# Optimization experiments

Measured on AMD Instinct MI355X. Metric: run time of the kernel, lower is better.

Reference implementation:

```python
import jax, jax.numpy as jnp
import numpy as np

H = 8            # num_heads
A = 8            # num_atlas
LAMBDA_INIT = 0.8
EPS = 1e-5


def setup_inputs() -> dict:
    key = jax.random.key(0)
    ks = jax.random.split(key, 12)
    B, N, D = 16, 2048, 1024
    d = D // (2 * H)  # half-head dim = 64
    sc = D ** -0.5
    return {
        "x": jax.random.normal(ks[0], (B, N, D), jnp.float32),
        "atlas_q": jax.random.normal(ks[1], (A, D), jnp.float32) * 0.02,  # learned atlas query tokens
        "Wq": jax.random.normal(ks[2], (D, D), jnp.float32) * sc,
        "Wk": jax.random.normal(ks[3], (D, D), jnp.float32) * sc,
        "Wv": jax.random.normal(ks[4], (D, D), jnp.float32) * sc,
        "Wo": jax.random.normal(ks[5], (D, D), jnp.float32) * sc,
        "rms_w": jnp.ones((2 * d,), jnp.float32),
        "Whead": jax.random.normal(ks[6], (D, 1), jnp.float32) * sc,
        "lq1": jax.random.normal(ks[7], (d,), jnp.float32) * 0.1,
        "lk1": jax.random.normal(ks[8], (d,), jnp.float32) * 0.1,
        "lq2": jax.random.normal(ks[9], (d,), jnp.float32) * 0.1,
        "lk2": jax.random.normal(ks[10], (d,), jnp.float32) * 0.1,
    }


def reference(x, atlas_q, Wq, Wk, Wv, Wo, rms_w, Whead, lq1, lk1, lq2, lk2):
    B, N, D = x.shape
    d = D // (2 * H)
    # projections (bias-free, as in DIFF transformer)
    q = (atlas_q @ Wq).reshape(A, 2 * H, d)          # [A, 2H, d]
    k = (x @ Wk).reshape(B, N, 2 * H, d)             # [B, N, 2H, d]
    v = (x @ Wv).reshape(B, N, H, 2 * d)             # [B, N, H, 2d]
    # attention scores: atlas queries attend over tokens
    scores = jnp.einsum("ahd,bnhd->bhan", q, k) * (d ** -0.5)  # [B, 2H, A, N]
    s = jax.nn.softmax(scores, axis=-1).reshape(B, H, 2, A, N)
    # differential lambda
    lam = jnp.exp(jnp.dot(lq1, lk1)) - jnp.exp(jnp.dot(lq2, lk2)) + LAMBDA_INIT
    diff = s[:, :, 0] - lam * s[:, :, 1]             # [B, H, A, N]
    out = jnp.einsum("bhan,bnhe->bahe", diff, v)     # [B, A, H, 2d]
    # per-head RMSNorm, scaled by (1 - lambda_init)
    out = out * jax.lax.rsqrt(jnp.mean(out * out, axis=-1, keepdims=True) + EPS)
    out = out * rms_w * (1.0 - LAMBDA_INIT)
    out = out.reshape(B, A, D) @ Wo                  # [B, A, D]
    logits = (out @ Whead)[..., 0]                   # [B, A] routing logits
    return logits
```

## Files before the change

kernel.cpp:

```cpp
#include <hip/hip_runtime.h>
#include <hip/hip_bf16.h>
#include <cstdint>

#define BB 16
#define NN 2048
#define DD 1024
#define HH 8
#define AA 8
#define CC 128
#define DH 64
#define TD 128
#define LAMBDA_INIT 0.8f
#define EPS_ 1e-5f

typedef short short8 __attribute__((ext_vector_type(8)));
typedef float f32x4  __attribute__((ext_vector_type(4)));

static __device__ __forceinline__ ushort f2bf(float f) {
    uint32_t u = __float_as_uint(f);
    return (ushort)((u + 0x8000u) >> 16);
}

static constexpr size_t OFF_QPROJP = 0;
static constexpr size_t OFF_M2     = 65536;
static constexpr size_t OFF_LAM    = 131072;
static constexpr size_t OFF_WOH    = 131136;
static constexpr size_t OFF_SC     = 132160;
static constexpr size_t OFF_DIFFB  = OFF_SC + 4194304;

__global__ __launch_bounds__(256) void k_setup(const float* __restrict__ atlas_q,
                                               const float* __restrict__ Wq,
                                               const float* __restrict__ Wo,
                                               const float* __restrict__ Whead,
                                               const float* __restrict__ lq1,
                                               const float* __restrict__ lk1,
                                               const float* __restrict__ lq2,
                                               const float* __restrict__ lk2,
                                               float* __restrict__ qprojp,
                                               float* __restrict__ woh,
                                               float* __restrict__ lam) {
    int blk = blockIdx.x;
    int tid = threadIdx.x;
    if (blk < 128) {
        __shared__ float aqS[8][128];
        __shared__ float redS[4][8][64];
        int jt = blk >> 3, iq = blk & 7;
        if (tid < 128) {
#pragma unroll
            for (int a = 0; a < 8; ++a) aqS[a][tid] = atlas_q[a * DD + iq * 128 + tid];
        }
        __syncthreads();
        int jl = tid & 63, is = tid >> 6;
        float acc[8] = {};
        const float* wq = Wq + (size_t)(iq * 128 + is * 32) * DD + jt * 64 + jl;
#pragma unroll 8
        for (int ii = 0; ii < 32; ++ii) {
            float wv = wq[(size_t)ii * DD];
            int i = is * 32 + ii;
#pragma unroll
            for (int a = 0; a < 8; ++a) acc[a] = fmaf(aqS[a][i], wv, acc[a]);
        }
#pragma unroll
        for (int a = 0; a < 8; ++a) redS[is][a][jl] = acc[a];
        __syncthreads();
        if (tid < 64) {
#pragma unroll
            for (int a = 0; a < 8; ++a)
                qprojp[(size_t)iq * 8192 + a * 1024 + jt * 64 + tid] =
                    redS[0][a][tid] + redS[1][a][tid] + redS[2][a][tid] + redS[3][a][tid];
        }
    } else if (blk < 192) {
        int i0 = (blk - 128) * 16;
        int il = tid >> 4, jt = tid & 15;
        const float* row = Wo + (size_t)(i0 + il) * DD;
        float acc = 0.f;
#pragma unroll 4
        for (int u = 0; u < 16; ++u) {
            float4 r  = *(const float4*)(row + u * 64 + jt * 4);
            float4 wv = *(const float4*)(Whead + u * 64 + jt * 4);
            acc += r.x * wv.x + r.y * wv.y + r.z * wv.z + r.w * wv.w;
        }
#pragma unroll
        for (int off = 8; off; off >>= 1) acc += __shfl_down(acc, off);
        if ((tid & 15) == 0) woh[i0 + il] = acc;
    } else {
        if (tid < 64) {
            float p1 = lq1[tid] * lk1[tid];
            float p2 = lq2[tid] * lk2[tid];
#pragma unroll
            for (int off = 32; off; off >>= 1) {
                p1 += __shfl_down(p1, off);
                p2 += __shfl_down(p2, off);
            }
            if (tid == 0) *lam = expf(p1) - expf(p2) + LAMBDA_INIT;
        }
    }
}

__global__ __launch_bounds__(256) void k_m2(const float* __restrict__ qprojp,
                                            const float* __restrict__ Wk,
                                            ushort* __restrict__ M2) {
    __shared__ float qpS[8192];
    int jb = blockIdx.x;
    int tid = threadIdx.x;
#pragma unroll
    for (int e = 0; e < 32; ++e) {
        int idx = tid + e * 256;
        float s = 0.f;
#pragma unroll
        for (int iq = 0; iq < 8; ++iq) s += qprojp[(size_t)iq * 8192 + idx];
        qpS[idx] = s;
    }
    __syncthreads();
    int h2 = tid >> 4;
#pragma unroll
    for (int jr = 0; jr < 2; ++jr) {
        int j = jb * 2 + jr;
        float4 wv = *(const float4*)(Wk + (size_t)j * DD + tid * 4);
        float p[8];
#pragma unroll
        for (int a = 0; a < 8; ++a) {
            float4 q4 = *(const float4*)(&qpS[a * DD + tid * 4]);
            p[a] = q4.x * wv.x + q4.y * wv.y + q4.z * wv.z + q4.w * wv.w;
        }
#pragma unroll
        for (int off = 8; off; off >>= 1)
#pragma unroll
            for (int a = 0; a < 8; ++a) p[a] += __shfl_down(p[a], off);
        if ((tid & 15) == 0) {
#pragma unroll
            for (int a = 0; a < 8; ++a)
                M2[(size_t)(h2 * 8 + a) * DD + j] = f2bf(p[a] * 0.125f);
        }
    }
}

__global__ __launch_bounds__(256, 4) void k_scores(const float* __restrict__ x,
                                                   const ushort* __restrict__ M2,
                                                   float* __restrict__ scores) {
    int b = blockIdx.x, nt = blockIdx.y;
    int tid = threadIdx.x;
    int lane = tid & 63, w = tid >> 6;
    int wn = w >> 1, wc = w & 1;
    int l15 = lane & 15, kg = lane >> 4;
    int n = nt * 32 + wn * 16 + l15;
    const float* xr = x + ((size_t)b * NN + n) * DD + kg * 8;

    f32x4 acc[4] = {};
    float4 pa0 = *(const float4*)(xr);
    float4 pa1 = *(const float4*)(xr + 4);
    float4 pa2 = *(const float4*)(xr + 32);
    float4 pa3 = *(const float4*)(xr + 36);

    for (int j0 = 0; j0 < DD; j0 += 64) {
        float4 ca0 = pa0, ca1 = pa1, ca2 = pa2, ca3 = pa3;
        if (j0 < DD - 64) {
            pa0 = *(const float4*)(xr + j0 + 64);
            pa1 = *(const float4*)(xr + j0 + 68);
            pa2 = *(const float4*)(xr + j0 + 96);
            pa3 = *(const float4*)(xr + j0 + 100);
        }
        short8 av0, av1;
        av0[0] = (short)f2bf(ca0.x); av0[1] = (short)f2bf(ca0.y);
        av0[2] = (short)f2bf(ca0.z); av0[3] = (short)f2bf(ca0.w);
        av0[4] = (short)f2bf(ca1.x); av0[5] = (short)f2bf(ca1.y);
        av0[6] = (short)f2bf(ca1.z); av0[7] = (short)f2bf(ca1.w);
        av1[0] = (short)f2bf(ca2.x); av1[1] = (short)f2bf(ca2.y);
        av1[2] = (short)f2bf(ca2.z); av1[3] = (short)f2bf(ca2.w);
        av1[4] = (short)f2bf(ca3.x); av1[5] = (short)f2bf(ca3.y);
        av1[6] = (short)f2bf(ca3.z); av1[7] = (short)f2bf(ca3.w);
        const ushort* m2b = M2 + (size_t)(wc * 64) * DD + j0 + kg * 8;
#pragma unroll
        for (int ct = 0; ct < 4; ++ct) {
            uint4 b0 = *(const uint4*)(m2b + (size_t)(ct * 16 + l15) * DD);
            uint4 b1 = *(const uint4*)(m2b + (size_t)(ct * 16 + l15) * DD + 32);
            acc[ct] = __builtin_amdgcn_mfma_f32_16x16x32_bf16(
                av0, __builtin_bit_cast(short8, b0), acc[ct], 0, 0, 0);
            acc[ct] = __builtin_amdgcn_mfma_f32_16x16x32_bf16(
                av1, __builtin_bit_cast(short8, b1), acc[ct], 0, 0, 0);
        }
    }
#pragma unroll
    for (int ct = 0; ct < 4; ++ct) {
        int c = wc * 64 + ct * 16 + l15;
        float4 o = {acc[ct][0], acc[ct][1], acc[ct][2], acc[ct][3]};
        *(float4*)(scores + ((size_t)b * CC + c) * NN + nt * 32 + wn * 16 + kg * 4) = o;
    }
}

__global__ __launch_bounds__(256) void k_softdiff(const float* __restrict__ scores,
                                                  const float* __restrict__ lam_p,
                                                  ushort* __restrict__ diffb) {
    int blk = blockIdx.x;
    int b = blk >> 6, h = (blk >> 3) & 7, a = blk & 7;
    int tid = threadIdx.x;
    const float* r0 = scores + ((size_t)b * CC + (2 * h) * AA + a) * NN;
    const float* r1 = scores + ((size_t)b * CC + (2 * h + 1) * AA + a) * NN;
    float v0[8], v1[8];
    float m0 = -1e30f, m1 = -1e30f;
#pragma unroll
    for (int k = 0; k < 8; ++k) {
        v0[k] = r0[tid + k * 256];
        v1[k] = r1[tid + k * 256];
        m0 = fmaxf(m0, v0[k]); m1 = fmaxf(m1, v1[k]);
    }
    __shared__ float redm[4][2];
    __shared__ float reds[4][2];
    int w = tid >> 6, lane = tid & 63;
#pragma unroll
    for (int off = 32; off; off >>= 1) {
        m0 = fmaxf(m0, __shfl_down(m0, off));
        m1 = fmaxf(m1, __shfl_down(m1, off));
    }
    if (lane == 0) { redm[w][0] = m0; redm[w][1] = m1; }
    __syncthreads();
    m0 = fmaxf(fmaxf(redm[0][0], redm[1][0]), fmaxf(redm[2][0], redm[3][0]));
    m1 = fmaxf(fmaxf(redm[0][1], redm[1][1]), fmaxf(redm[2][1], redm[3][1]));
    float s0 = 0.f, s1 = 0.f;
#pragma unroll
    for (int k = 0; k < 8; ++k) {
        v0[k] = expf(v0[k] - m0); s0 += v0[k];
        v1[k] = expf(v1[k] - m1); s1 += v1[k];
    }
#pragma unroll
    for (int off = 32; off; off >>= 1) {
        s0 += __shfl_down(s0, off);
        s1 += __shfl_down(s1, off);
    }
    if (lane == 0) { reds[w][0] = s0; reds[w][1] = s1; }
    __syncthreads();
    s0 = reds[0][0] + reds[1][0] + reds[2][0] + reds[3][0];
    s1 = reds[0][1] + reds[1][1] + reds[2][1] + reds[3][1];
    float lam = *lam_p;
    float inv0 = 1.f / s0;
    float inv1 = lam / s1;
    ushort* drow = diffb + ((size_t)b * 64 + a * 8 + h) * NN;
#pragma unroll
    for (int k = 0; k < 8; ++k)
        drow[tid + k * 256] = f2bf(v0[k] * inv0 - v1[k] * inv1);
}

__global__ __launch_bounds__(256, 4) void k_agg(const float* __restrict__ x,
                                                const ushort* __restrict__ diffb,
                                                float* __restrict__ aggp) {
    __shared__ ushort xT[64 * 32];
    int b = blockIdx.x, jt = blockIdx.y, sk = blockIdx.z;
    int j0 = jt * 64;
    int tid = threadIdx.x;
    int nl = tid & 31, jc = tid >> 5;
    int lane = tid & 63, w = tid >> 6;
    int l15 = lane & 15, kg = lane >> 4;
    int nbase = sk * 512;

    f32x4 acc[4] = {};
    const float* xb = x + (size_t)b * NN * DD;
    const ushort* drow = diffb + (size_t)b * 64 * NN;

    const float* s0p = xb + (size_t)(nbase + nl) * DD + j0 + jc * 8;
    float4 p0 = *(const float4*)(s0p);
    float4 p1 = *(const float4*)(s0p + 4);
    uint4 an[4];
#pragma unroll
    for (int rt = 0; rt < 4; ++rt)
        an[rt] = *(const uint4*)(drow + (size_t)(rt * 16 + l15) * NN + nbase + kg * 8);

    for (int stp = 0; stp < 16; ++stp) {
        int jb = jc * 8;
        xT[(jb + 0) * 32 + nl] = f2bf(p0.x);
        xT[(jb + 1) * 32 + nl] = f2bf(p0.y);
        xT[(jb + 2) * 32 + nl] = f2bf(p0.z);
        xT[(jb + 3) * 32 + nl] = f2bf(p0.w);
        xT[(jb + 4) * 32 + nl] = f2bf(p1.x);
        xT[(jb + 5) * 32 + nl] = f2bf(p1.y);
        xT[(jb + 6) * 32 + nl] = f2bf(p1.z);
        xT[(jb + 7) * 32 + nl] = f2bf(p1.w);
        uint4 ac0 = an[0], ac1 = an[1], ac2 = an[2], ac3 = an[3];
        if (stp < 15) {
            int n1 = nbase + (stp + 1) * 32;
            const float* sp = xb + (size_t)(n1 + nl) * DD + j0 + jc * 8;
            p0 = *(const float4*)(sp);
            p1 = *(const float4*)(sp + 4);
#pragma unroll
            for (int rt = 0; rt < 4; ++rt)
                an[rt] = *(const uint4*)(drow + (size_t)(rt * 16 + l15) * NN + n1 + kg * 8);
        }
        __syncthreads();
        short8 bv = __builtin_bit_cast(short8,
            *(const uint4*)(xT + (size_t)(w * 16 + l15) * 32 + kg * 8));
        acc[0] = __builtin_amdgcn_mfma_f32_16x16x32_bf16(__builtin_bit_cast(short8, ac0), bv, acc[0], 0, 0, 0);
        acc[1] = __builtin_amdgcn_mfma_f32_16x16x32_bf16(__builtin_bit_cast(short8, ac1), bv, acc[1], 0, 0, 0);
        acc[2] = __builtin_amdgcn_mfma_f32_16x16x32_bf16(__builtin_bit_cast(short8, ac2), bv, acc[2], 0, 0, 0);
        acc[3] = __builtin_amdgcn_mfma_f32_16x16x32_bf16(__builtin_bit_cast(short8, ac3), bv, acc[3], 0, 0, 0);
        __syncthreads();
    }
    int jj = j0 + w * 16 + l15;
#pragma unroll
    for (int rt = 0; rt < 4; ++rt) {
#pragma unroll
        for (int reg = 0; reg < 4; ++reg) {
            int r = rt * 16 + kg * 4 + reg;
            aggp[(((size_t)sk * BB + b) * 64 + r) * DD + jj] = acc[rt][reg];
        }
    }
}

__global__ __launch_bounds__(256) void k_yp(const float* __restrict__ aggp,
                                            const float* __restrict__ Wv,
                                            float* __restrict__ Y) {
    __shared__ float As[8][32];
    __shared__ float Ws[32][128];
    int h = blockIdx.x, rt = blockIdx.y;
    int tid = threadIdx.x;
    int rl = tid >> 5, te = tid & 31;
    int row0 = rt * 8;
    float a0 = 0.f, a1 = 0.f, a2 = 0.f, a3 = 0.f;
    for (int j0 = 0; j0 < DD; j0 += 32) {
        {
            int r = row0 + rl;
            int b_ = r >> 3, a_ = r & 7;
            size_t base = (((size_t)b_ * 64) + a_ * 8 + h) * DD + j0 + te;
            const size_t skS = (size_t)BB * 64 * DD;
            As[rl][te] = aggp[base] + aggp[base + skS] + aggp[base + 2 * skS] + aggp[base + 3 * skS];
        }
#pragma unroll
        for (int t = 0; t < 4; ++t) {
            int f4 = tid + t * 256;
            int jj = f4 >> 5, e4 = (f4 & 31) * 4;
            *(float4*)(&Ws[jj][e4]) = *(const float4*)(Wv + (size_t)(j0 + jj) * DD + h * TD + e4);
        }
        __syncthreads();
#pragma unroll
        for (int jj = 0; jj < 32; ++jj) {
            float av = As[rl][jj];
            float4 w4 = *(const float4*)(&Ws[jj][te * 4]);
            a0 = fmaf(av, w4.x, a0);
            a1 = fmaf(av, w4.y, a1);
            a2 = fmaf(av, w4.z, a2);
            a3 = fmaf(av, w4.w, a3);
        }
        __syncthreads();
    }
    float4 o = {a0, a1, a2, a3};
    *(float4*)(Y + (size_t)(row0 + rl) * DD + h * TD + te * 4) = o;
}

__global__ __launch_bounds__(256) void k_logits(const float* __restrict__ Y,
                                                const float* __restrict__ rms_w,
                                                const float* __restrict__ woh,
                                                float* __restrict__ logits) {
    int row = blockIdx.x;
    int tid = threadIdx.x;
    int w = tid >> 6, lane = tid & 63;
    __shared__ float hss[8];
    __shared__ float red[4];
    float y[4];
    if (tid < 8) hss[tid] = 0.f;
    __syncthreads();
#pragma unroll
    for (int k = 0; k < 4; ++k) {
        int p = k * 256 + tid;
        y[k] = Y[(size_t)row * DD + p];
        float s = y[k] * y[k];
#pragma unroll
        for (int off = 32; off; off >>= 1) s += __shfl_down(s, off);
        if (lane == 0) atomicAdd(&hss[(k * 256 + w * 64) >> 7], s);
    }
    __syncthreads();
    float val = 0.f;
#pragma unroll
    for (int k = 0; k < 4; ++k) {
        int p = k * 256 + tid;
        int hh = p >> 7, e = p & 127;
        float rs = rsqrtf(hss[hh] * (1.f / 128.f) + EPS_);
        val += y[k] * rs * rms_w[e] * (1.f - LAMBDA_INIT) * woh[p];
    }
#pragma unroll
    for (int off = 32; off; off >>= 1) val += __shfl_down(val, off);
    if (lane == 0) red[w] = val;
    __syncthreads();
    if (tid == 0) logits[row] = red[0] + red[1] + red[2] + red[3];
}

extern "C" void kernel_launch(void* const* d_in, const int* in_sizes, int n_in,
                              void* d_out, int out_size, void* d_ws, size_t ws_size,
                              hipStream_t stream) {
    (void)in_sizes; (void)n_in; (void)out_size; (void)ws_size;
    const float* x       = (const float*)d_in[0];
    const float* atlas_q = (const float*)d_in[1];
    const float* Wq      = (const float*)d_in[2];
    const float* Wk      = (const float*)d_in[3];
    const float* Wv      = (const float*)d_in[4];
    const float* Wo      = (const float*)d_in[5];
    const float* rms_w   = (const float*)d_in[6];
    const float* Whead   = (const float*)d_in[7];
    const float* lq1     = (const float*)d_in[8];
    const float* lk1     = (const float*)d_in[9];
    const float* lq2     = (const float*)d_in[10];
    const float* lk2     = (const float*)d_in[11];
    float* out = (float*)d_out;
    float* ws  = (float*)d_ws;

    float*  qprojp = ws + OFF_QPROJP;
    ushort* M2     = (ushort*)(ws + OFF_M2);
    float*  lam    = ws + OFF_LAM;
    float*  woh    = ws + OFF_WOH;
    float*  scores = ws + OFF_SC;
    float*  aggp   = ws + OFF_SC;
    ushort* diffb  = (ushort*)(ws + OFF_DIFFB);
    float*  Y      = ws + OFF_DIFFB;

    hipLaunchKernelGGL(k_setup,    dim3(193),       dim3(256), 0, stream,
                       atlas_q, Wq, Wo, Whead, lq1, lk1, lq2, lk2, qprojp, woh, lam);
    hipLaunchKernelGGL(k_m2,       dim3(512),       dim3(256), 0, stream, qprojp, Wk, M2);
    hipLaunchKernelGGL(k_scores,   dim3(16, 64),    dim3(256), 0, stream, x, M2, scores);
    hipLaunchKernelGGL(k_softdiff, dim3(1024),      dim3(256), 0, stream, scores, lam, diffb);
    hipLaunchKernelGGL(k_agg,      dim3(16, 16, 4), dim3(256), 0, stream, x, diffb, aggp);
    hipLaunchKernelGGL(k_yp,       dim3(8, 16),     dim3(256), 0, stream, aggp, Wv, Y);
    hipLaunchKernelGGL(k_logits,   dim3(128),       dim3(256), 0, stream, Y, rms_w, woh, out);
}
```

Baseline: 380.8 us.

## Stage x and M2 tiles through double-buffered LDS and split k_yp over j

k_scores now handles 64 token rows per block. It stages both the bf16-converted x tile and the M2 tile in padded, double-buffered shared memory, so each wave reuses the shared A and B fragments across 4x2 MFMA tiles instead of reloading M2 from global memory per wave. k_agg moves to 64-token chunks with a double-buffered transpose buffer and register prefetch of both operands, halving the number of barriers per MFMA. k_yp is split four ways along the reduction dimension for more parallelism, with the partial sums combined in k_logits. The changes add shared memory use and register pressure, which may lower occupancy.

Result: faster. 308.7 us (-18.9%).

```diff
diff --git a/kernel.cpp b/kernel.cpp
--- a/kernel.cpp
+++ b/kernel.cpp
@@ -19,6 +19,9 @@
 static __device__ __forceinline__ ushort f2bf(float f) {
     uint32_t u = __float_as_uint(f);
     return (ushort)((u + 0x8000u) >> 16);
+}
+static __device__ __forceinline__ uint pack2(float a, float b) {
+    return (uint)f2bf(a) | ((uint)f2bf(b) << 16);
 }
 
 static constexpr size_t OFF_QPROJP = 0;
@@ -135,57 +138,83 @@
     }
 }
 
-__global__ __launch_bounds__(256, 4) void k_scores(const float* __restrict__ x,
-                                                   const ushort* __restrict__ M2,
-                                                   float* __restrict__ scores) {
+__global__ __launch_bounds__(256) void k_scores(const float* __restrict__ x,
+                                                const ushort* __restrict__ M2,
+                                                float* __restrict__ scores) {
+    __shared__ ushort xs[2][64][72];
+    __shared__ ushort ms[2][128][72];
     int b = blockIdx.x, nt = blockIdx.y;
     int tid = threadIdx.x;
     int lane = tid & 63, w = tid >> 6;
-    int wn = w >> 1, wc = w & 1;
     int l15 = lane & 15, kg = lane >> 4;
-    int n = nt * 32 + wn * 16 + l15;
-    const float* xr = x + ((size_t)b * NN + n) * DD + kg * 8;
-
-    f32x4 acc[4] = {};
-    float4 pa0 = *(const float4*)(xr);
-    float4 pa1 = *(const float4*)(xr + 4);
-    float4 pa2 = *(const float4*)(xr + 32);
-    float4 pa3 = *(const float4*)(xr + 36);
-
-    for (int j0 = 0; j0 < DD; j0 += 64) {
-        float4 ca0 = pa0, ca1 = pa1, ca2 = pa2, ca3 = pa3;
-        if (j0 < DD - 64) {
-            pa0 = *(const float4*)(xr + j0 + 64);
-            pa1 = *(const float4*)(xr + j0 + 68);
-            pa2 = *(const float4*)(xr + j0 + 96);
-            pa3 = *(const float4*)(xr + j0 + 100);
-        }
-        short8 av0, av1;
-        av0[0] = (short)f2bf(ca0.x); av0[1] = (short)f2bf(ca0.y);
-        av0[2] = (short)f2bf(ca0.z); av0[3] = (short)f2bf(ca0.w);
-        av0[4] = (short)f2bf(ca1.x); av0[5] = (short)f2bf(ca1.y);
-        av0[6] = (short)f2bf(ca1.z); av0[7] = (short)f2bf(ca1.w);
-        av1[0] = (short)f2bf(ca2.x); av1[1] = (short)f2bf(ca2.y);
-        av1[2] = (short)f2bf(ca2.z); av1[3] = (short)f2bf(ca2.w);
-        av1[4] = (short)f2bf(ca3.x); av1[5] = (short)f2bf(ca3.y);
-        av1[6] = (short)f2bf(ca3.z); av1[7] = (short)f2bf(ca3.w);
-        const ushort* m2b = M2 + (size_t)(wc * 64) * DD + j0 + kg * 8;
-#pragma unroll
-        for (int ct = 0; ct < 4; ++ct) {
-            uint4 b0 = *(const uint4*)(m2b + (size_t)(ct * 16 + l15) * DD);
-            uint4 b1 = *(const uint4*)(m2b + (size_t)(ct * 16 + l15) * DD + 32);
-            acc[ct] = __builtin_amdgcn_mfma_f32_16x16x32_bf16(
-                av0, __builtin_bit_cast(short8, b0), acc[ct], 0, 0, 0);
-            acc[ct] = __builtin_amdgcn_mfma_f32_16x16x32_bf16(
-                av1, __builtin_bit_cast(short8, b1), acc[ct], 0, 0, 0);
-        }
-    }
-#pragma unroll
-    for (int ct = 0; ct < 4; ++ct) {
-        int c = wc * 64 + ct * 16 + l15;
-        float4 o = {acc[ct][0], acc[ct][1], acc[ct][2], acc[ct][3]};
-        *(float4*)(scores + ((size_t)b * CC + c) * NN + nt * 32 + wn * 16 + kg * 4) = o;
-    }
+    int xr4 = tid >> 4, xq = tid & 15;
+    int mr  = tid >> 3, mq = tid & 7;
+    const float* xbase = x + ((size_t)b * NN + nt * 64) * DD;
+
+    f32x4 acc[4][2] = {};
+
+    float4 RXa[4], RXb[4];
+    uint4  RMa[4], RMb[4];
+
+    auto LOAD = [&](float4 (&RX)[4], uint4 (&RM)[4], int j0) {
+#pragma unroll
+        for (int p = 0; p < 4; ++p)
+            RX[p] = *(const float4*)(xbase + (size_t)(p * 16 + xr4) * DD + j0 + xq * 4);
+#pragma unroll
+        for (int p = 0; p < 4; ++p)
+            RM[p] = *(const uint4*)(M2 + (size_t)(p * 32 + mr) * DD + j0 + mq * 8);
+    };
+    auto WRITE = [&](int buf, float4 (&RX)[4], uint4 (&RM)[4]) {
+#pragma unroll
+        for (int p = 0; p < 4; ++p) {
+            uint* d = (uint*)&xs[buf][p * 16 + xr4][xq * 4];
+            d[0] = pack2(RX[p].x, RX[p].y);
+            d[1] = pack2(RX[p].z, RX[p].w);
+        }
+#pragma unroll
+        for (int p = 0; p < 4; ++p) {
+            uint* d = (uint*)&ms[buf][p * 32 + mr][mq * 8];
+            d[0] = RM[p].x; d[1] = RM[p].y; d[2] = RM[p].z; d[3] = RM[p].w;
+        }
+    };
+    auto COMPUTE = [&](int buf) {
+#pragma unroll
+        for (int ks = 0; ks < 2; ++ks) {
+            short8 av[4];
+#pragma unroll
+            for (int nt2 = 0; nt2 < 4; ++nt2)
+                av[nt2] = *(const short8*)&xs[buf][nt2 * 16 + l15][ks * 32 + kg * 8];
+#pragma unroll
+            for (int ct2 = 0; ct2 < 2; ++ct2) {
+                short8 bv = *(const short8*)&ms[buf][w * 32 + ct2 * 16 + l15][ks * 32 + kg * 8];
+#pragma unroll
+                for (int nt2 = 0; nt2 < 4; ++nt2)
+                    acc[nt2][ct2] = __builtin_amdgcn_mfma_f32_16x16x32_bf16(av[nt2], bv, acc[nt2][ct2], 0, 0, 0);
+            }
+        }
+    };
+
+    LOAD(RXa, RMa, 0);
+#pragma unroll 1
+    for (int cc = 0; cc < 8; ++cc) {
+        int c0 = cc * 2;
+        LOAD(RXb, RMb, (c0 + 1) * 64);
+        WRITE(0, RXa, RMa);
+        __syncthreads();
+        COMPUTE(0);
+        if (c0 + 2 < 16) LOAD(RXa, RMa, (c0 + 2) * 64);
+        WRITE(1, RXb, RMb);
+        __syncthreads();
+        COMPUTE(1);
+    }
+#pragma unroll
+    for (int nt2 = 0; nt2 < 4; ++nt2)
+#pragma unroll
+        for (int ct2 = 0; ct2 < 2; ++ct2) {
+            int c = w * 32 + ct2 * 16 + l15;
+            float4 o = {acc[nt2][ct2][0], acc[nt2][ct2][1], acc[nt2][ct2][2], acc[nt2][ct2][3]};
+            *(float4*)(scores + ((size_t)b * CC + c) * NN + nt * 64 + nt2 * 16 + kg * 4) = o;
+        }
 }
 
 __global__ __launch_bounds__(256) void k_softdiff(const float* __restrict__ scores,
@@ -240,81 +269,99 @@
         drow[tid + k * 256] = f2bf(v0[k] * inv0 - v1[k] * inv1);
 }
 
-__global__ __launch_bounds__(256, 4) void k_agg(const float* __restrict__ x,
+__global__ __launch_bounds__(256, 3) void k_agg(const float* __restrict__ x,
                                                 const ushort* __restrict__ diffb,
                                                 float* __restrict__ aggp) {
-    __shared__ ushort xT[64 * 32];
+    __shared__ ushort xT[2][64][72];
     int b = blockIdx.x, jt = blockIdx.y, sk = blockIdx.z;
-    int j0 = jt * 64;
-    int tid = threadIdx.x;
-    int nl = tid & 31, jc = tid >> 5;
+    int j0 = jt * 64, nbase = sk * 512;
+    int tid = threadIdx.x;
+    int nr = tid >> 3, jq = tid & 7;
     int lane = tid & 63, w = tid >> 6;
     int l15 = lane & 15, kg = lane >> 4;
-    int nbase = sk * 512;
-
-    f32x4 acc[4] = {};
     const float* xb = x + (size_t)b * NN * DD;
     const ushort* drow = diffb + (size_t)b * 64 * NN;
 
-    const float* s0p = xb + (size_t)(nbase + nl) * DD + j0 + jc * 8;
-    float4 p0 = *(const float4*)(s0p);
-    float4 p1 = *(const float4*)(s0p + 4);
-    uint4 an[4];
+    f32x4 acc[4] = {};
+
+    float4 PXa[2][2], PXb[2][2];
+    uint4  ANa[4][2], ANb[4][2];
+
+    auto LOADX = [&](float4 (&P)[2][2], int c) {
+#pragma unroll
+        for (int p = 0; p < 2; ++p) {
+            const float* s = xb + (size_t)(nbase + c * 64 + p * 32 + nr) * DD + j0 + jq * 8;
+            P[p][0] = *(const float4*)(s);
+            P[p][1] = *(const float4*)(s + 4);
+        }
+    };
+    auto LOADA = [&](uint4 (&A)[4][2], int c) {
+#pragma unroll
+        for (int rt = 0; rt < 4; ++rt)
+#pragma unroll
+            for (int ks = 0; ks < 2; ++ks)
+                A[rt][ks] = *(const uint4*)(drow + (size_t)(rt * 16 + l15) * NN
+                                            + nbase + c * 64 + ks * 32 + kg * 8);
+    };
+    auto WRITE = [&](int buf, float4 (&P)[2][2]) {
+#pragma unroll
+        for (int p = 0; p < 2; ++p) {
+            int n = p * 32 + nr;
+            xT[buf][jq * 8 + 0][n] = f2bf(P[p][0].x);
+            xT[buf][jq * 8 + 1][n] = f2bf(P[p][0].y);
+            xT[buf][jq * 8 + 2][n] = f2bf(P[p][0].z);
+            xT[buf][jq * 8 + 3][n] = f2bf(P[p][0].w);
+            xT[buf][jq * 8 + 4][n] = f2bf(P[p][1].x);
+            xT[buf][jq * 8 + 5][n] = f2bf(P[p][1].y);
+            xT[buf][jq * 8 + 6][n] = f2bf(P[p][1].z);
+            xT[buf][jq * 8 + 7][n] = f2bf(P[p][1].w);
+        }
+    };
+    auto COMPUTE = [&](int buf, uint4 (&A)[4][2]) {
+#pragma unroll
+        for (int ks = 0; ks < 2; ++ks) {
+            short8 bv = *(const short8*)&xT[buf][w * 16 + l15][ks * 32 + kg * 8];
+#pragma unroll
+            for (int rt = 0; rt < 4; ++rt)
+                acc[rt] = __builtin_amdgcn_mfma_f32_16x16x32_bf16(
+                    __builtin_bit_cast(short8, A[rt][ks]), bv, acc[rt], 0, 0, 0);
+        }
+    };
+
+    LOADX(PXa, 0); LOADA(ANa, 0);
+#pragma unroll 1
+    for (int cc = 0; cc < 4; ++cc) {
+        int c0 = cc * 2;
+        LOADX(PXb, c0 + 1); LOADA(ANb, c0 + 1);
+        WRITE(0, PXa);
+        __syncthreads();
+        COMPUTE(0, ANa);
+        if (c0 + 2 < 8) { LOADX(PXa, c0 + 2); LOADA(ANa, c0 + 2); }
+        WRITE(1, PXb);
+        __syncthreads();
+        COMPUTE(1, ANb);
+    }
+    int jj = j0 + w * 16 + l15;
 #pragma unroll
     for (int rt = 0; rt < 4; ++rt)
-        an[rt] = *(const uint4*)(drow + (size_t)(rt * 16 + l15) * NN + nbase + kg * 8);
-
-    for (int stp = 0; stp < 16; ++stp) {
-        int jb = jc * 8;
-        xT[(jb + 0) * 32 + nl] = f2bf(p0.x);
-        xT[(jb + 1) * 32 + nl] = f2bf(p0.y);
-        xT[(jb + 2) * 32 + nl] = f2bf(p0.z);
-        xT[(jb + 3) * 32 + nl] = f2bf(p0.w);
-        xT[(jb + 4) * 32 + nl] = f2bf(p1.x);
-        xT[(jb + 5) * 32 + nl] = f2bf(p1.y);
-        xT[(jb + 6) * 32 + nl] = f2bf(p1.z);
-        xT[(jb + 7) * 32 + nl] = f2bf(p1.w);
-        uint4 ac0 = an[0], ac1 = an[1], ac2 = an[2], ac3 = an[3];
-        if (stp < 15) {
-            int n1 = nbase + (stp + 1) * 32;
-            const float* sp = xb + (size_t)(n1 + nl) * DD + j0 + jc * 8;
-            p0 = *(const float4*)(sp);
-            p1 = *(const float4*)(sp + 4);
-#pragma unroll
-            for (int rt = 0; rt < 4; ++rt)
-                an[rt] = *(const uint4*)(drow + (size_t)(rt * 16 + l15) * NN + n1 + kg * 8);
-        }
-        __syncthreads();
-        short8 bv = __builtin_bit_cast(short8,
-            *(const uint4*)(xT + (size_t)(w * 16 + l15) * 32 + kg * 8));
-        acc[0] = __builtin_amdgcn_mfma_f32_16x16x32_bf16(__builtin_bit_cast(short8, ac0), bv, acc[0], 0, 0, 0);
-        acc[1] = __builtin_amdgcn_mfma_f32_16x16x32_bf16(__builtin_bit_cast(short8, ac1), bv, acc[1], 0, 0, 0);
-        acc[2] = __builtin_amdgcn_mfma_f32_16x16x32_bf16(__builtin_bit_cast(short8, ac2), bv, acc[2], 0, 0, 0);
-        acc[3] = __builtin_amdgcn_mfma_f32_16x16x32_bf16(__builtin_bit_cast(short8, ac3), bv, acc[3], 0, 0, 0);
-        __syncthreads();
-    }
-    int jj = j0 + w * 16 + l15;
-#pragma unroll
-    for (int rt = 0; rt < 4; ++rt) {
 #pragma unroll
         for (int reg = 0; reg < 4; ++reg) {
             int r = rt * 16 + kg * 4 + reg;
             aggp[(((size_t)sk * BB + b) * 64 + r) * DD + jj] = acc[rt][reg];
         }
-    }
 }
 
 __global__ __launch_bounds__(256) void k_yp(const float* __restrict__ aggp,
                                             const float* __restrict__ Wv,
-                                            float* __restrict__ Y) {
+                                            float* __restrict__ ypp) {
     __shared__ float As[8][32];
     __shared__ float Ws[32][128];
-    int h = blockIdx.x, rt = blockIdx.y;
+    int h = blockIdx.x, rt = blockIdx.y, jp = blockIdx.z;
     int tid = threadIdx.x;
     int rl = tid >> 5, te = tid & 31;
     int row0 = rt * 8;
     float a0 = 0.f, a1 = 0.f, a2 = 0.f, a3 = 0.f;
-    for (int j0 = 0; j0 < DD; j0 += 32) {
+    for (int j0 = jp * 256; j0 < jp * 256 + 256; j0 += 32) {
         {
             int r = row0 + rl;
             int b_ = r >> 3, a_ = r & 7;
@@ -341,10 +388,10 @@
         __syncthreads();
     }
     float4 o = {a0, a1, a2, a3};
-    *(float4*)(Y + (size_t)(row0 + rl) * DD + h * TD + te * 4) = o;
-}
-
-__global__ __launch_bounds__(256) void k_logits(const float* __restrict__ Y,
+    *(float4*)(ypp + ((size_t)jp * 128 + row0 + rl) * DD + h * TD + te * 4) = o;
+}
+
+__global__ __launch_bounds__(256) void k_logits(const float* __restrict__ ypp,
                                                 const float* __restrict__ rms_w,
                                                 const float* __restrict__ woh,
                                                 float* __restrict__ logits) {
@@ -359,7 +406,9 @@
 #pragma unroll
     for (int k = 0; k < 4; ++k) {
         int p = k * 256 + tid;
-        y[k] = Y[(size_t)row * DD + p];
+        const size_t jS = (size_t)128 * DD;
+        size_t base = (size_t)row * DD + p;
+        y[k] = ypp[base] + ypp[base + jS] + ypp[base + 2 * jS] + ypp[base + 3 * jS];
         float s = y[k] * y[k];
 #pragma unroll
         for (int off = 32; off; off >>= 1) s += __shfl_down(s, off);
@@ -407,14 +456,14 @@
     float*  scores = ws + OFF_SC;
     float*  aggp   = ws + OFF_SC;
     ushort* diffb  = (ushort*)(ws + OFF_DIFFB);
-    float*  Y      = ws + OFF_DIFFB;
-
-    hipLaunchKernelGGL(k_setup,    dim3(193),       dim3(256), 0, stream,
+    float*  ypp    = ws + OFF_DIFFB;
+
+    hipLaunchKernelGGL(k_setup,    dim3(193),        dim3(256), 0, stream,
                        atlas_q, Wq, Wo, Whead, lq1, lk1, lq2, lk2, qprojp, woh, lam);
-    hipLaunchKernelGGL(k_m2,       dim3(512),       dim3(256), 0, stream, qprojp, Wk, M2);
-    hipLaunchKernelGGL(k_scores,   dim3(16, 64),    dim3(256), 0, stream, x, M2, scores);
-    hipLaunchKernelGGL(k_softdiff, dim3(1024),      dim3(256), 0, stream, scores, lam, diffb);
-    hipLaunchKernelGGL(k_agg,      dim3(16, 16, 4), dim3(256), 0, stream, x, diffb, aggp);
-    hipLaunchKernelGGL(k_yp,       dim3(8, 16),     dim3(256), 0, stream, aggp, Wv, Y);
-    hipLaunchKernelGGL(k_logits,   dim3(128),       dim3(256), 0, stream, Y, rms_w, woh, out);
-}
+    hipLaunchKernelGGL(k_m2,       dim3(512),        dim3(256), 0, stream, qprojp, Wk, M2);
+    hipLaunchKernelGGL(k_scores,   dim3(16, 32),     dim3(256), 0, stream, x, M2, scores);
+    hipLaunchKernelGGL(k_softdiff, dim3(1024),       dim3(256), 0, stream, scores, lam, diffb);
+    hipLaunchKernelGGL(k_agg,      dim3(16, 16, 4),  dim3(256), 0, stream, x, diffb, aggp);
+    hipLaunchKernelGGL(k_yp,       dim3(8, 16, 4),   dim3(256), 0, stream, aggp, Wv, ypp);
+    hipLaunchKernelGGL(k_logits,   dim3(128),        dim3(256), 0, stream, ypp, rms_w, woh, out);
+}
```
